# Kernel tuning notes

Measured on AMD Instinct MI355X. Metric: run time of the kernel, lower is better.

Reference implementation:

```python
import jax, jax.numpy as jnp
import numpy as np

GATE_SLOPE = 5.0
BRANCH_BREAK = 0.5

def setup_inputs() -> dict:
    key = jax.random.key(0)
    ks = jax.random.split(key, 6)
    B, I, O, N = 1024, 64, 64, 16
    x = jax.random.normal(ks[0], (B, I), dtype=jnp.float32)
    k = jax.random.uniform(ks[1], (I, O, N), dtype=jnp.float32) * 2 + 0.5
    Ec = jax.random.uniform(ks[2], (I, O, N), dtype=jnp.float32) * 2 + 0.5
    Ps = jax.random.uniform(ks[3], (I, O, N), dtype=jnp.float32) * 1.5 + 0.5
    bias = jax.random.normal(ks[4], (I, O, N), dtype=jnp.float32) * 0.1
    coef = jax.random.normal(ks[5], (I, O, N), dtype=jnp.float32)
    return {"x": x, "k": k, "Ec": Ec, "Ps": Ps, "bias": bias, "coef": coef}

def reference(x, k, Ec, Ps, bias, coef):
    # prev_x buffer starts at zeros and is overwritten (detached) with the
    # previous sample each loop iteration -> prev row = shifted x.
    prev = jnp.concatenate([jnp.zeros((1, x.shape[1]), x.dtype), x[:-1]], axis=0)
    dx = x - jax.lax.stop_gradient(prev)                  # (B, I)
    g = jax.nn.sigmoid(GATE_SLOPE * dx)
    branch = (g > BRANCH_BREAK).astype(x.dtype)[:, :, None, None]  # (B, I, 1, 1)
    xe = x[:, :, None, None]                              # (B, I, 1, 1)
    # Ps * (2*sigmoid(k*(x -/+ Ec)) - 1)
    P_up = Ps * (2.0 * jax.nn.sigmoid(k * (xe - Ec)) - 1.0)   # (B, I, O, N)
    P_down = Ps * (2.0 * jax.nn.sigmoid(k * (xe + Ec)) - 1.0)
    basis = branch * P_up + (1.0 - branch) * P_down + bias
    # weighted sum over in_dim and num_basis -> (B, O)
    return jnp.einsum('bion,ion->bo', basis, coef)
```

## Files before the change

kernel.cpp:

```cpp
#include <hip/hip_runtime.h>
#include <hip/hip_bf16.h>


#define LOG2E 1.44269504088896340736f
#define B_DIM 1024
#define I_DIM 64
#define O_DIM 64
#define N_DIM 16
#define ION (I_DIM * O_DIM * N_DIM)

__device__ __forceinline__ float ex2(float x) {
#if __has_builtin(__builtin_amdgcn_exp2f)
  return __builtin_amdgcn_exp2f(x);
#else
  return exp2f(x);
#endif
}

__global__ void zero_c0(float* C0) { C0[threadIdx.x] = 0.0f; }

__global__ __launch_bounds__(256) void transform_k(
    const float* __restrict__ k, const float* __restrict__ Ec,
    const float* __restrict__ Ps, const float* __restrict__ bias,
    const float* __restrict__ coef, float4* __restrict__ P4,
    float* __restrict__ C0) {
  int idx = blockIdx.x * 256 + threadIdx.x;
  float kv = k[idx], ev = Ec[idx], pv = Ps[idx], bv = bias[idx], cv = coef[idx];
  float kk = -LOG2E * kv;
  float E  =  LOG2E * kv * ev;
  float A  =  2.0f * pv * cv;
  P4[idx] = make_float4(kk, E, A, 0.0f);
  float cpart = (bv - pv) * cv;
  #pragma unroll
  for (int off = 1; off < 16; off <<= 1)
    cpart += __shfl_xor(cpart, off, 64);
  if ((threadIdx.x & 15) == 0)
    atomicAdd(&C0[(idx >> 4) & (O_DIM - 1)], cpart);
}

__global__ __launch_bounds__(256) void out_init(const float* __restrict__ C0,
                                                float* __restrict__ out) {
  int gid = blockIdx.x * 256 + threadIdx.x;
  out[gid] = C0[gid & (O_DIM - 1)];
}

__global__ __launch_bounds__(256) void ferro_main(
    const float* __restrict__ x, const float4* __restrict__ P4,
    float* __restrict__ out) {
  int t  = threadIdx.x;
  int o  = t >> 2;
  int bs = t & 3;
  int ic = blockIdx.x & 15;
  int bc = blockIdx.x >> 4;
  int r0 = bc * 32 + bs * 8;

  float acc[8];
  #pragma unroll
  for (int j = 0; j < 8; ++j) acc[j] = 0.0f;

  for (int ii = 0; ii < 4; ++ii) {
    int i = ic * 4 + ii;
    float xv[9];
    xv[0] = (r0 == 0) ? 0.0f : x[(r0 - 1) * I_DIM + i];
    #pragma unroll
    for (int j = 0; j < 8; ++j) xv[j + 1] = x[(r0 + j) * I_DIM + i];
    bool br[8];
    #pragma unroll
    for (int j = 0; j < 8; ++j) br[j] = xv[j + 1] > xv[j];

    const float4* p = &P4[(i * O_DIM + o) * N_DIM];
    #pragma unroll
    for (int n = 0; n < N_DIM; ++n) {
      float4 pv = p[n];
      float kk = pv.x, E = pv.y, A = pv.z;
      #pragma unroll
      for (int j = 0; j < 8; ++j) {
        float e = br[j] ? E : -E;
        float z = fmaf(kk, xv[j + 1], e);
        float tt = ex2(z);
        float r  = __builtin_amdgcn_rcpf(1.0f + tt);
        acc[j] = fmaf(A, r, acc[j]);
      }
    }
  }

  #pragma unroll
  for (int j = 0; j < 8; ++j)
    atomicAdd(&out[(r0 + j) * O_DIM + o], acc[j]);
}

extern "C" void kernel_launch(void* const* d_in, const int* in_sizes, int n_in,
                              void* d_out, int out_size, void* d_ws, size_t ws_size,
                              hipStream_t stream) {
  const float* x    = (const float*)d_in[0];
  const float* k    = (const float*)d_in[1];
  const float* Ec   = (const float*)d_in[2];
  const float* Ps   = (const float*)d_in[3];
  const float* bias = (const float*)d_in[4];
  const float* coef = (const float*)d_in[5];
  float* out = (float*)d_out;

  float4* P4 = (float4*)d_ws;
  float*  C0 = (float*)((char*)d_ws + (size_t)ION * sizeof(float4));

  hipLaunchKernelGGL(zero_c0,    dim3(1),   dim3(64),  0, stream, C0);
  hipLaunchKernelGGL(transform_k, dim3(ION / 256), dim3(256), 0, stream,
                     k, Ec, Ps, bias, coef, P4, C0);
  hipLaunchKernelGGL(out_init,   dim3(ION / 256), dim3(256), 0, stream, C0, out);
  hipLaunchKernelGGL(ferro_main, dim3(512), dim3(256), 0, stream, x, P4, out);
}
```

Measured before the change: 91.88 us.

## Coalesce parameter layout and replace output atomics with partial-sum reduction

Parameters are repacked so consecutive output channels are contiguous, and the bias/coef constant is folded into the fourth float4 lane instead of a separate atomic-reduced C0 buffer. The main kernel now maps threads to output channel within a wavefront with 4 rows each over twice as many blocks. It writes per-input-chunk partial sums to a workspace, and a new reduce kernel sums them, replacing global atomics and the zero/init kernels. This trades atomic contention and strided parameter loads for an extra partial-sum buffer round-trip and less register reuse of each parameter load.

```diff
diff --git a/kernel.cpp b/kernel.cpp
--- a/kernel.cpp
+++ b/kernel.cpp
@@ -7,7 +7,7 @@
 #define I_DIM 64
 #define O_DIM 64
 #define N_DIM 16
-#define ION (I_DIM * O_DIM * N_DIM)
+#define ION   65536
 
 __device__ __forceinline__ float ex2(float x) {
 #if __has_builtin(__builtin_amdgcn_exp2f)
@@ -17,76 +17,74 @@
 #endif
 }
 
-__global__ void zero_c0(float* C0) { C0[threadIdx.x] = 0.0f; }
-
-__global__ __launch_bounds__(256) void transform_k(
+__global__ __launch_bounds__(256) void prep(
     const float* __restrict__ k, const float* __restrict__ Ec,
     const float* __restrict__ Ps, const float* __restrict__ bias,
-    const float* __restrict__ coef, float4* __restrict__ P4,
-    float* __restrict__ C0) {
+    const float* __restrict__ coef, float4* __restrict__ Q) {
   int idx = blockIdx.x * 256 + threadIdx.x;
+  int i = idx >> 10, o = (idx >> 4) & 63, n = idx & 15;
   float kv = k[idx], ev = Ec[idx], pv = Ps[idx], bv = bias[idx], cv = coef[idx];
   float kk = -LOG2E * kv;
   float E  =  LOG2E * kv * ev;
   float A  =  2.0f * pv * cv;
-  P4[idx] = make_float4(kk, E, A, 0.0f);
-  float cpart = (bv - pv) * cv;
-  #pragma unroll
-  for (int off = 1; off < 16; off <<= 1)
-    cpart += __shfl_xor(cpart, off, 64);
-  if ((threadIdx.x & 15) == 0)
-    atomicAdd(&C0[(idx >> 4) & (O_DIM - 1)], cpart);
-}
-
-__global__ __launch_bounds__(256) void out_init(const float* __restrict__ C0,
-                                                float* __restrict__ out) {
-  int gid = blockIdx.x * 256 + threadIdx.x;
-  out[gid] = C0[gid & (O_DIM - 1)];
+  float W  = (bv - pv) * cv;
+  Q[(i * N_DIM + n) * O_DIM + o] = make_float4(kk, E, A, W);
 }
 
 __global__ __launch_bounds__(256) void ferro_main(
-    const float* __restrict__ x, const float4* __restrict__ P4,
-    float* __restrict__ out) {
+    const float* __restrict__ x, const float4* __restrict__ Q,
+    float* __restrict__ part) {
   int t  = threadIdx.x;
-  int o  = t >> 2;
-  int bs = t & 3;
+  int o  = t & 63;
+  int w  = t >> 6;
   int ic = blockIdx.x & 15;
   int bc = blockIdx.x >> 4;
-  int r0 = bc * 32 + bs * 8;
+  int r0 = bc * 16 + w * 4;
 
-  float acc[8];
-  #pragma unroll
-  for (int j = 0; j < 8; ++j) acc[j] = 0.0f;
+  float acc0 = 0.f, acc1 = 0.f, acc2 = 0.f, acc3 = 0.f, wsum = 0.f;
 
+  #pragma unroll 1
   for (int ii = 0; ii < 4; ++ii) {
     int i = ic * 4 + ii;
-    float xv[9];
-    xv[0] = (r0 == 0) ? 0.0f : x[(r0 - 1) * I_DIM + i];
-    #pragma unroll
-    for (int j = 0; j < 8; ++j) xv[j + 1] = x[(r0 + j) * I_DIM + i];
-    bool br[8];
-    #pragma unroll
-    for (int j = 0; j < 8; ++j) br[j] = xv[j + 1] > xv[j];
+    float xm = (r0 == 0) ? 0.0f : x[(r0 - 1) * I_DIM + i];
+    float x0 = x[(r0 + 0) * I_DIM + i];
+    float x1 = x[(r0 + 1) * I_DIM + i];
+    float x2 = x[(r0 + 2) * I_DIM + i];
+    float x3 = x[(r0 + 3) * I_DIM + i];
+    bool b0 = x0 > xm, b1 = x1 > x0, b2 = x2 > x1, b3 = x3 > x2;
 
-    const float4* p = &P4[(i * O_DIM + o) * N_DIM];
+    const float4* q = Q + (i * N_DIM) * O_DIM + o;
     #pragma unroll
     for (int n = 0; n < N_DIM; ++n) {
-      float4 pv = p[n];
-      float kk = pv.x, E = pv.y, A = pv.z;
-      #pragma unroll
-      for (int j = 0; j < 8; ++j) {
-        float e = br[j] ? E : -E;
-        float z = fmaf(kk, xv[j + 1], e);
-        float tt = ex2(z);
-        float r  = __builtin_amdgcn_rcpf(1.0f + tt);
-        acc[j] = fmaf(A, r, acc[j]);
-      }
+      float4 p = q[n * O_DIM];
+      float E = p.y, nE = -p.y;
+      wsum += p.w;
+      float e0 = b0 ? E : nE, e1 = b1 ? E : nE, e2 = b2 ? E : nE, e3 = b3 ? E : nE;
+      float s0 = __builtin_amdgcn_rcpf(1.0f + ex2(fmaf(p.x, x0, e0)));
+      float s1 = __builtin_amdgcn_rcpf(1.0f + ex2(fmaf(p.x, x1, e1)));
+      float s2 = __builtin_amdgcn_rcpf(1.0f + ex2(fmaf(p.x, x2, e2)));
+      float s3 = __builtin_amdgcn_rcpf(1.0f + ex2(fmaf(p.x, x3, e3)));
+      acc0 = fmaf(p.z, s0, acc0);
+      acc1 = fmaf(p.z, s1, acc1);
+      acc2 = fmaf(p.z, s2, acc2);
+      acc3 = fmaf(p.z, s3, acc3);
     }
   }
 
+  float* dst = part + ((size_t)ic * B_DIM + r0) * O_DIM + o;
+  dst[0 * O_DIM] = acc0 + wsum;
+  dst[1 * O_DIM] = acc1 + wsum;
+  dst[2 * O_DIM] = acc2 + wsum;
+  dst[3 * O_DIM] = acc3 + wsum;
+}
+
+__global__ __launch_bounds__(256) void reduce_k(
+    const float* __restrict__ part, float* __restrict__ out) {
+  int gid = blockIdx.x * 256 + threadIdx.x;
+  float s = 0.f;
   #pragma unroll
-  for (int j = 0; j < 8; ++j)
-    atomicAdd(&out[(r0 + j) * O_DIM + o], acc[j]);
+  for (int ic = 0; ic < 16; ++ic) s += part[ic * (B_DIM * O_DIM) + gid];
+  out[gid] = s;
 }
 
 extern "C" void kernel_launch(void* const* d_in, const int* in_sizes, int n_in,
@@ -100,12 +98,12 @@
   const float* coef = (const float*)d_in[5];
   float* out = (float*)d_out;
 
-  float4* P4 = (float4*)d_ws;
-  float*  C0 = (float*)((char*)d_ws + (size_t)ION * sizeof(float4));
+  float4* Q    = (float4*)d_ws;
+  float*  part = (float*)((char*)d_ws + (size_t)ION * sizeof(float4));
 
-  hipLaunchKernelGGL(zero_c0,    dim3(1),   dim3(64),  0, stream, C0);
-  hipLaunchKernelGGL(transform_k, dim3(ION / 256), dim3(256), 0, stream,
-                     k, Ec, Ps, bias, coef, P4, C0);
-  hipLaunchKernelGGL(out_init,   dim3(ION / 256), dim3(256), 0, stream, C0, out);
-  hipLaunchKernelGGL(ferro_main, dim3(512), dim3(256), 0, stream, x, P4, out);
+  hipLaunchKernelGGL(prep,       dim3(ION / 256), dim3(256), 0, stream,
+                     k, Ec, Ps, bias, coef, Q);
+  hipLaunchKernelGGL(ferro_main, dim3(1024),      dim3(256), 0, stream, x, Q, part);
+  hipLaunchKernelGGL(reduce_k,   dim3(B_DIM * O_DIM / 256), dim3(256), 0, stream,
+                     part, out);
 }
```

New measurement: 83.71 us. -8.9%, faster.
